# Performance work log

Hardware: AMD Instinct MI355X
Metric: run time of the kernel (lower is better)

## Reference

```python
import jax, jax.numpy as jnp
import numpy as np

EPS = 1e-8
TAU = 1.0
ROLL_TOPK = 20
FINAL_TOPK = 20


def _ln(x, g, b):
    mu = x.mean(-1, keepdims=True)
    var = ((x - mu) ** 2).mean(-1, keepdims=True)
    return (x - mu) / jnp.sqrt(var + 1e-5) * g + b


def _row_norm(A, pm):
    A = A * pm
    return A / (A.sum(-1, keepdims=True) + EPS)


def _topk_sparsify(A, k, pm):
    thr = jax.lax.top_k(A, k)[0][..., -1:]  # per-row k-th largest
    return _row_norm(jnp.where(A >= thr, A, 0.0), pm)


def setup_inputs():
    key = jax.random.key(0)
    ks = iter(jax.random.split(key, 48))
    B, N, Din, Dh, T, R, Bn = 4, 2000, 128, 256, 64, 16, 64
    def w(shape, s=0.02):
        return jax.random.normal(next(ks), shape, jnp.float32) * s
    inp = dict(
        X=jax.random.normal(next(ks), (B, N, Din), jnp.float32),
        mask=jnp.ones((B, N), dtype=bool),
        history=jax.random.normal(next(ks), (B, N, T), jnp.float32),
        enc_ln_g=jnp.ones((Din,)), enc_ln_b=jnp.zeros((Din,)),
        enc_w1=w((Din, Bn)), enc_b1=jnp.zeros((Bn,)),
        enc_w2=w((Bn, Din)), enc_b2=jnp.zeros((Din,)),
        proj_w=w((Din, Dh)), proj_b=jnp.zeros((Dh,)),
        fdg_B=w((R, Din), 0.1),
        mix_logit=jnp.asarray(np.log(0.7 / 0.3), dtype=jnp.float32),
        gblk_ln_g=jnp.ones((Dh,)), gblk_ln_b=jnp.zeros((Dh,)),
        gblk_w1=w((Dh, Dh)), gblk_b1=jnp.zeros((Dh,)),
        gblk_w2=w((Dh, Dh)), gblk_b2=jnp.zeros((Dh,)),
        head_ln_g=jnp.ones((Dh,)), head_ln_b=jnp.zeros((Dh,)),
        head_w=w((Dh, 1)), head_b=jnp.zeros((1,)),
    )
    for i in range(2):  # residual_layers=2
        inp[f'blk{i}_ln_g'] = jnp.ones((Dh,))
        inp[f'blk{i}_ln_b'] = jnp.zeros((Dh,))
        inp[f'blk{i}_w1'] = w((Dh, Dh))
        inp[f'blk{i}_b1'] = jnp.zeros((Dh,))
        inp[f'blk{i}_w2'] = w((Dh, Dh))
        inp[f'blk{i}_b2'] = jnp.zeros((Dh,))
    return inp


def _forward(X, mask, history, enc_ln_g, enc_ln_b, enc_w1, enc_b1, enc_w2, enc_b2,
             proj_w, proj_b,
             blk0_ln_g, blk0_ln_b, blk0_w1, blk0_b1, blk0_w2, blk0_b2,
             blk1_ln_g, blk1_ln_b, blk1_w1, blk1_b1, blk1_w2, blk1_b2,
             fdg_B, mix_logit,
             gblk_ln_g, gblk_ln_b, gblk_w1, gblk_b1, gblk_w2, gblk_b2,
             head_ln_g, head_ln_b, head_w, head_b):
    m = mask.astype(X.dtype)[..., None]                      # [B,N,1]
    pm = (mask[:, :, None] & mask[:, None, :]).astype(X.dtype)  # [B,N,N]
    # FeatureBottleneck encoder (residual down-up projection)
    h = _ln(X, enc_ln_g, enc_ln_b)
    Xm = (X + jax.nn.gelu(h @ enc_w1 + enc_b1) @ enc_w2 + enc_b2) * m
    hid = (Xm @ proj_w + proj_b) * m
    # ResidualMLP blocks
    for (g, bb, w1, b1, w2, b2) in ((blk0_ln_g, blk0_ln_b, blk0_w1, blk0_b1, blk0_w2, blk0_b2),
                                    (blk1_ln_g, blk1_ln_b, blk1_w1, blk1_b1, blk1_w2, blk1_b2)):
        hh = _ln(hid, g, bb)
        hid = (hid + jax.nn.gelu(hh @ w1 + b1) @ w2 + b2) * m
    # FDG: low-rank cosine-similarity graph with temperature softmax
    Z = Xm @ fdg_B.T                                          # [B,N,R]
    Zn = Z / (jnp.linalg.norm(Z, axis=-1, keepdims=True) + EPS)
    S = jnp.einsum('bnr,bmr->bnm', Zn, Zn) / TAU
    A_fdg = jax.nn.softmax(jnp.where(pm > 0, S, -1e9), axis=-1) * pm
    # Rolling correlation graph from history returns
    Hc = history - history.mean(-1, keepdims=True)
    Hn = Hc / (Hc.std(-1, keepdims=True) + EPS)
    C = jnp.einsum('bnt,bmt->bnm', Hn, Hn) / history.shape[-1]
    A_roll = _topk_sparsify(_row_norm(jax.nn.relu(C), pm), ROLL_TOPK, pm)
    # Mix -> row-normalize -> final top-k sparsify
    mix = jax.nn.sigmoid(mix_logit)
    A = _row_norm(mix * A_fdg + (1.0 - mix) * A_roll, pm)
    A = _topk_sparsify(A, FINAL_TOPK, pm)
    # GraphResidual block: aggregate then MLP with residual
    hh = _ln(hid, gblk_ln_g, gblk_ln_b)
    msg = jnp.einsum('bnm,bmd->bnd', A, hh)
    hid = (hid + jax.nn.gelu(msg @ gblk_w1 + gblk_b1) @ gblk_w2 + gblk_b2) * m
    # Head
    y = (jax.nn.gelu(_ln(hid, head_ln_g, head_ln_b)) @ head_w + head_b)[..., 0]
    return jnp.where(mask, y, 0.0)


def reference(X, mask, history, enc_ln_g, enc_ln_b, enc_w1, enc_b1, enc_w2, enc_b2,
              proj_w, proj_b,
              blk0_ln_g, blk0_ln_b, blk0_w1, blk0_b1, blk0_w2, blk0_b2,
              blk1_ln_g, blk1_ln_b, blk1_w1, blk1_b1, blk1_w2, blk1_b2,
              fdg_B, mix_logit,
              gblk_ln_g, gblk_ln_b, gblk_w1, gblk_b1, gblk_w2, gblk_b2,
              head_ln_g, head_ln_b, head_w, head_b):
    return _forward(X, mask, history, enc_ln_g, enc_ln_b, enc_w1, enc_b1, enc_w2, enc_b2,
                    proj_w, proj_b,
                    blk0_ln_g, blk0_ln_b, blk0_w1, blk0_b1, blk0_w2, blk0_b2,
                    blk1_ln_g, blk1_ln_b, blk1_w1, blk1_b1, blk1_w2, blk1_b2,
                    fdg_B, mix_logit,
                    gblk_ln_g, gblk_ln_b, gblk_w1, gblk_b1, gblk_w2, gblk_b2,
                    head_ln_g, head_ln_b, head_w, head_b)
```

## Files before the change

kernel.cpp:

```cpp
#include <hip/hip_runtime.h>
#include <math.h>

#define NB 4
#define N 2000
#define DIN 128
#define DH 256
#define NROWS (NB*N)
#define EPSF 1e-8f

typedef __attribute__((ext_vector_type(8))) short bf16x8;
typedef __attribute__((ext_vector_type(4))) float f32x4;


__device__ __forceinline__ float gelu_t(float x){
    float z = 0.7978845608028654f * fmaf(0.044715f * x * x, x, x);
    z = fminf(fmaxf(z, -20.f), 20.f);
    float e = __expf(2.f * z);
    return 0.5f * x * (1.f + (e - 1.f) / (e + 1.f));
}

__device__ __forceinline__ unsigned short f2bf(float f){
    unsigned u = __float_as_uint(f);
    return (unsigned short)((u + 0x7FFFu + ((u >> 16) & 1u)) >> 16);
}

__device__ __forceinline__ float wave_sort64_desc(float v){
    const int lane = threadIdx.x & 63;
    #pragma unroll
    for (int k = 2; k <= 64; k <<= 1){
        #pragma unroll
        for (int j = k >> 1; j >= 1; j >>= 1){
            float o = __shfl_xor(v, j, 64);
            bool keepMax = ((lane & k) == 0) == ((lane & j) == 0);
            v = keepMax ? fmaxf(v, o) : fminf(v, o);
        }
    }
    return v;
}

__device__ __forceinline__ void sort128_desc(float &v0, float &v1){
    const int lane = threadIdx.x & 63;
    #pragma unroll
    for (int k = 2; k <= 128; k <<= 1){
        #pragma unroll
        for (int j = k >> 1; j >= 2; j >>= 1){
            int lj = j >> 1;
            float o0 = __shfl_xor(v0, lj, 64);
            float o1 = __shfl_xor(v1, lj, 64);
            int idx0 = 2*lane, idx1 = 2*lane + 1;
            bool km0 = ((idx0 & k) == 0) == ((idx0 & j) == 0);
            bool km1 = ((idx1 & k) == 0) == ((idx1 & j) == 0);
            v0 = km0 ? fmaxf(v0, o0) : fminf(v0, o0);
            v1 = km1 ? fmaxf(v1, o1) : fminf(v1, o1);
        }
        {
            bool up = (((2*lane) & k) == 0);
            float a = fmaxf(v0, v1), b = fminf(v0, v1);
            v0 = up ? a : b;
            v1 = up ? b : a;
        }
    }
}

__device__ __forceinline__ float wave_topk20_slow32(const float (&v)[32]){
    float cur = 1e30f, kth = 0.f;
    int consumed = 0;
    for (int it = 0; it < 20; ++it){
        if (consumed >= 20) break;
        float bm = -3.f;
        #pragma unroll
        for (int i = 0; i < 32; ++i){ if (v[i] < cur) bm = fmaxf(bm, v[i]); }
        #pragma unroll
        for (int mm = 1; mm < 64; mm <<= 1) bm = fmaxf(bm, __shfl_xor(bm, mm, 64));
        int c = 0;
        #pragma unroll
        for (int i = 0; i < 32; ++i) c += (v[i] == bm) ? 1 : 0;
        #pragma unroll
        for (int mm = 1; mm < 64; mm <<= 1) c += __shfl_xor(c, mm, 64);
        consumed += c;
        kth = bm;
        cur = bm;
    }
    return kth;
}

__device__ __forceinline__ float wave_topk20_sync(const float (&v)[32], float* cl){
    const int lane = threadIdx.x & 63;
    float mx = v[0];
    #pragma unroll
    for (int i = 1; i < 32; ++i) mx = fmaxf(mx, v[i]);
    float sm = wave_sort64_desc(mx);
    float u = __shfl(sm, 19, 64);
    int cnt = 0;
    #pragma unroll
    for (int i = 0; i < 32; ++i) cnt += (v[i] >= u) ? 1 : 0;
    int incl = cnt;
    #pragma unroll
    for (int s = 1; s < 64; s <<= 1){
        int o = __shfl_up(incl, s, 64);
        if (lane >= s) incl += o;
    }
    const int total = __shfl(incl, 63, 64);
    const bool fast = (total <= 128);
    if (fast){
        int offs = incl - cnt;
        #pragma unroll
        for (int i = 0; i < 32; ++i){
            if (v[i] >= u) cl[offs++] = v[i];
        }
    }
    __syncthreads();
    float kth;
    if (fast){
        float c0 = (2*lane     < total) ? cl[2*lane]     : -3.f;
        float c1 = (2*lane + 1 < total) ? cl[2*lane + 1] : -3.f;
        sort128_desc(c0, c1);
        kth = __shfl(c1, 9, 64);
    } else {
        kth = wave_topk20_slow32(v);
    }
    __syncthreads();
    return kth;
}

__device__ __forceinline__ void mfma_gemm16(
    const unsigned short (*__restrict__ sA)[264], const unsigned short* __restrict__ Wt,
    int l15, int hi, int cbase, f32x4 acc[4])
{
    bf16x8 a[8];
    #pragma unroll
    for (int kb = 0; kb < 8; ++kb)
        a[kb] = *(const bf16x8*)&sA[l15][kb*32 + hi*8];
    __syncthreads();
    const unsigned short* wp0 = Wt + (size_t)(cbase      + l15)*256 + hi*8;
    const unsigned short* wp1 = Wt + (size_t)(cbase + 16 + l15)*256 + hi*8;
    const unsigned short* wp2 = Wt + (size_t)(cbase + 32 + l15)*256 + hi*8;
    const unsigned short* wp3 = Wt + (size_t)(cbase + 48 + l15)*256 + hi*8;
    #pragma unroll
    for (int kb = 0; kb < 8; ++kb){
        bf16x8 b0 = *(const bf16x8*)(wp0 + kb*32);
        bf16x8 b1 = *(const bf16x8*)(wp1 + kb*32);
        bf16x8 b2 = *(const bf16x8*)(wp2 + kb*32);
        bf16x8 b3 = *(const bf16x8*)(wp3 + kb*32);
        acc[0] = __builtin_amdgcn_mfma_f32_16x16x32_bf16(a[kb], b0, acc[0], 0, 0, 0);
        acc[1] = __builtin_amdgcn_mfma_f32_16x16x32_bf16(a[kb], b1, acc[1], 0, 0, 0);
        acc[2] = __builtin_amdgcn_mfma_f32_16x16x32_bf16(a[kb], b2, acc[2], 0, 0, 0);
        acc[3] = __builtin_amdgcn_mfma_f32_16x16x32_bf16(a[kb], b3, acc[3], 0, 0, 0);
    }
}


__global__ __launch_bounds__(256) void k_wcvt(
    const float* __restrict__ w10, const float* __restrict__ w20,
    const float* __restrict__ w11, const float* __restrict__ w21,
    const float* __restrict__ gw1, const float* __restrict__ gw2,
    unsigned short* __restrict__ Wt)
{
    __shared__ float t[32][33];
    const int m = blockIdx.z;
    const float* W = (m==0)?w10:(m==1)?w20:(m==2)?w11:(m==3)?w21:(m==4)?gw1:gw2;
    unsigned short* out = Wt + (size_t)m*65536;
    const int k0 = blockIdx.y*32, c0 = blockIdx.x*32;
    const int tx = threadIdx.x & 31, ty = threadIdx.x >> 5;
    #pragma unroll
    for (int j = 0; j < 4; ++j){
        int k = ty*4 + j;
        t[k][tx] = W[(size_t)(k0+k)*256 + c0+tx];
    }
    __syncthreads();
    #pragma unroll
    for (int j = 0; j < 4; ++j){
        int c = ty*4 + j;
        out[(size_t)(c0+c)*256 + k0+tx] = f2bf(t[tx][c]);
    }
}

__global__ __launch_bounds__(256) void k_enc(
    const float* __restrict__ X,
    const float* __restrict__ lg, const float* __restrict__ lb,
    const float* __restrict__ w1, const float* __restrict__ b1,
    const float* __restrict__ w2, const float* __restrict__ b2,
    const float* __restrict__ pw, const float* __restrict__ pb,
    const float* __restrict__ fB,
    float* __restrict__ hid, float* __restrict__ Zn)
{
    __shared__ float sH[8][132];
    __shared__ float sT[8][68];
    __shared__ float sXm[8][132];
    const int tid = threadIdx.x;
    const int lane = tid & 63;
    const int wave = tid >> 6;
    const int rg = wave * 2;
    const int row0 = blockIdx.x * 8;
    const int cx = lane * 2;
    float2 x0 = *(const float2*)(X + (size_t)(row0+rg  )*128 + cx);
    float2 x1 = *(const float2*)(X + (size_t)(row0+rg+1)*128 + cx);
    {
        float sa = x0.x + x0.y, sb = x1.x + x1.y;
        float qa = x0.x*x0.x + x0.y*x0.y, qb = x1.x*x1.x + x1.y*x1.y;
        #pragma unroll
        for (int m = 1; m < 64; m <<= 1){
            sa += __shfl_xor(sa, m, 64); sb += __shfl_xor(sb, m, 64);
            qa += __shfl_xor(qa, m, 64); qb += __shfl_xor(qb, m, 64);
        }
        float mua = sa*(1.f/128.f), mub = sb*(1.f/128.f);
        float rsa = rsqrtf(qa*(1.f/128.f) - mua*mua + 1e-5f);
        float rsb = rsqrtf(qb*(1.f/128.f) - mub*mub + 1e-5f);
        float2 gg = *(const float2*)(lg + cx);
        float2 bb = *(const float2*)(lb + cx);
        sH[rg  ][cx] = (x0.x - mua)*rsa*gg.x + bb.x;
        sH[rg  ][cx+1] = (x0.y - mua)*rsa*gg.y + bb.y;
        sH[rg+1][cx] = (x1.x - mub)*rsb*gg.x + bb.x;
        sH[rg+1][cx+1] = (x1.y - mub)*rsb*gg.y + bb.y;
    }
    __syncthreads();
    {
        float a0 = 0.f, a1 = 0.f;
        #pragma unroll 4
        for (int k = 0; k < 128; ++k){
            float h0 = sH[rg][k], h1 = sH[rg+1][k];
            float wk = w1[k*64 + lane];
            a0 = fmaf(h0, wk, a0);
            a1 = fmaf(h1, wk, a1);
        }
        float bb = b1[lane];
        sT[rg  ][lane] = gelu_t(a0 + bb);
        sT[rg+1][lane] = gelu_t(a1 + bb);
    }
    __syncthreads();
    {
        float p0x=0.f,p0y=0.f,p1x=0.f,p1y=0.f;
        #pragma unroll 4
        for (int k = 0; k < 64; ++k){
            float t0 = sT[rg][k], t1 = sT[rg+1][k];
            float2 w = *(const float2*)(w2 + k*128 + cx);
            p0x = fmaf(t0, w.x, p0x); p0y = fmaf(t0, w.y, p0y);
            p1x = fmaf(t1, w.x, p1x); p1y = fmaf(t1, w.y, p1y);
        }
        float2 bb = *(const float2*)(b2 + cx);
        sXm[rg  ][cx]   = x0.x + p0x + bb.x;
        sXm[rg  ][cx+1] = x0.y + p0y + bb.y;
        sXm[rg+1][cx]   = x1.x + p1x + bb.x;
        sXm[rg+1][cx+1] = x1.y + p1y + bb.y;
    }
    __syncthreads();
    {
        const int ri = lane >> 4;
        const int wc = wave*64 + (lane & 15)*4;
        float a0[4] = {0,0,0,0}, a1[4] = {0,0,0,0};
        #pragma unroll 4
        for (int k = 0; k < 128; ++k){
            float h0 = sXm[ri*2][k], h1 = sXm[ri*2+1][k];
            float4 w = *(const float4*)(pw + k*256 + wc);
            a0[0]=fmaf(h0,w.x,a0[0]); a0[1]=fmaf(h0,w.y,a0[1]); a0[2]=fmaf(h0,w.z,a0[2]); a0[3]=fmaf(h0,w.w,a0[3]);
            a1[0]=fmaf(h1,w.x,a1[0]); a1[1]=fmaf(h1,w.y,a1[1]); a1[2]=fmaf(h1,w.z,a1[2]); a1[3]=fmaf(h1,w.w,a1[3]);
        }
        float4 bb = *(const float4*)(pb + wc);
        float4 o0 = make_float4(a0[0]+bb.x, a0[1]+bb.y, a0[2]+bb.z, a0[3]+bb.w);
        float4 o1 = make_float4(a1[0]+bb.x, a1[1]+bb.y, a1[2]+bb.z, a1[3]+bb.w);
        *(float4*)(hid + (size_t)(row0+ri*2  )*256 + wc) = o0;
        *(float4*)(hid + (size_t)(row0+ri*2+1)*256 + wc) = o1;
    }
    if (tid < 128){
        const int r = tid >> 4, q = tid & 15;
        float z = 0.f;
        #pragma unroll 4
        for (int k = 0; k < 128; ++k) z = fmaf(sXm[r][k], fB[q*128 + k], z);
        float s2 = z*z;
        #pragma unroll
        for (int m = 1; m < 16; m <<= 1) s2 += __shfl_xor(s2, m, 64);
        Zn[(size_t)(row0 + r)*16 + q] = z / (sqrtf(s2) + EPSF);
    }
}

__global__ __launch_bounds__(256) void k_hist(const float* __restrict__ H, float* __restrict__ HnT)
{
    const int row  = blockIdx.x * 4 + (threadIdx.x >> 6);
    const int lane = threadIdx.x & 63;
    float v = H[(size_t)row*64 + lane];
    float s = v;
    #pragma unroll
    for (int mm = 1; mm < 64; mm <<= 1) s += __shfl_xor(s, mm, 64);
    float mu = s * (1.f/64.f);
    float d = v - mu;
    float s2 = d*d;
    #pragma unroll
    for (int mm = 1; mm < 64; mm <<= 1) s2 += __shfl_xor(s2, mm, 64);
    float sd = sqrtf(s2 * (1.f/64.f));
    const int b = row / N, nloc = row % N;
    HnT[(size_t)b*64*N + (size_t)lane*N + nloc] = d / ((sd + EPSF) * 8.f);
}

__global__ __launch_bounds__(256) void k_mlp2(
    float* __restrict__ hid, const unsigned short* __restrict__ Wtb,
    const float* __restrict__ g0, const float* __restrict__ be0,
    const float* __restrict__ b10, const float* __restrict__ b20,
    const float* __restrict__ g1, const float* __restrict__ be1,
    const float* __restrict__ b11, const float* __restrict__ b21,
    const float* __restrict__ hg, const float* __restrict__ hb,
    float* __restrict__ hh_out)
{
    __shared__ float sR[16][264];
    __shared__ unsigned short sA[16][264];
    const int tid = threadIdx.x;
    const int lane = tid & 63, wave = tid >> 6;
    const int l15 = lane & 15, hi = lane >> 4;
    const int cbase = wave * 64;
    const int row0 = blockIdx.x * 16;
    {
        const int r = tid >> 4, cb = (tid & 15) * 4;
        #pragma unroll
        for (int q = 0; q < 4; ++q)
            *(float4*)&sR[r][cb + q*64] =
                *(const float4*)(hid + (size_t)(row0+r)*256 + cb + q*64);
    }
    __syncthreads();
    #pragma unroll
    for (int it = 0; it < 2; ++it){
        const float* g  = it ? g1  : g0;
        const float* be = it ? be1 : be0;
        const float* B1 = it ? b11 : b10;
        const float* B2 = it ? b21 : b20;
        const unsigned short* W1 = Wtb + (size_t)(it ? 2 : 0)*65536;
        const unsigned short* W2 = Wtb + (size_t)(it ? 3 : 1)*65536;
        {
            float4 gg = *(const float4*)(g + lane*4);
            float4 bb = *(const float4*)(be + lane*4);
            #pragma unroll
            for (int j = 0; j < 4; ++j){
                const int r = wave*4 + j;
                float4 v = *(const float4*)&sR[r][lane*4];
                float s = v.x+v.y+v.z+v.w;
                float q = v.x*v.x+v.y*v.y+v.z*v.z+v.w*v.w;
                #pragma unroll
                for (int m = 1; m < 64; m <<= 1){
                    s += __shfl_xor(s, m, 64); q += __shfl_xor(q, m, 64);
                }
                float mu = s*(1.f/256.f);
                float rs = rsqrtf(q*(1.f/256.f) - mu*mu + 1e-5f);
                ushort4 o;
                o.x = f2bf((v.x-mu)*rs*gg.x+bb.x);
                o.y = f2bf((v.y-mu)*rs*gg.y+bb.y);
                o.z = f2bf((v.z-mu)*rs*gg.z+bb.z);
                o.w = f2bf((v.w-mu)*rs*gg.w+bb.w);
                *(ushort4*)&sA[r][lane*4] = o;
            }
        }
        __syncthreads();
        {
            f32x4 acc[4];
            #pragma unroll
            for (int t = 0; t < 4; ++t){ acc[t][0]=0.f; acc[t][1]=0.f; acc[t][2]=0.f; acc[t][3]=0.f; }
            mfma_gemm16(sA, W1, l15, hi, cbase, acc);
            #pragma unroll
            for (int t = 0; t < 4; ++t){
                int ct = cbase + t*16 + l15;
                float bbx = B1[ct];
                #pragma unroll
                for (int j = 0; j < 4; ++j)
                    sA[hi*4 + j][ct] = f2bf(gelu_t(acc[t][j] + bbx));
            }
        }
        __syncthreads();
        {
            f32x4 acc[4];
            #pragma unroll
            for (int t = 0; t < 4; ++t){ acc[t][0]=0.f; acc[t][1]=0.f; acc[t][2]=0.f; acc[t][3]=0.f; }
            mfma_gemm16(sA, W2, l15, hi, cbase, acc);
            #pragma unroll
            for (int t = 0; t < 4; ++t){
                int ct = cbase + t*16 + l15;
                float bbx = B2[ct];
                #pragma unroll
                for (int j = 0; j < 4; ++j)
                    sR[hi*4 + j][ct] += acc[t][j] + bbx;
            }
        }
        __syncthreads();
    }
    {
        const int r = tid >> 4, cb = (tid & 15) * 4;
        #pragma unroll
        for (int q = 0; q < 4; ++q)
            *(float4*)(hid + (size_t)(row0+r)*256 + cb + q*64) =
                *(const float4*)&sR[r][cb + q*64];
    }
    {
        float4 gg = *(const float4*)(hg + lane*4);
        float4 bb = *(const float4*)(hb + lane*4);
        #pragma unroll
        for (int j = 0; j < 4; ++j){
            const int r = wave*4 + j;
            float4 v = *(const float4*)&sR[r][lane*4];
            float s = v.x+v.y+v.z+v.w;
            float q = v.x*v.x+v.y*v.y+v.z*v.z+v.w*v.w;
            #pragma unroll
            for (int m = 1; m < 64; m <<= 1){
                s += __shfl_xor(s, m, 64); q += __shfl_xor(q, m, 64);
            }
            float mu = s*(1.f/256.f);
            float rs = rsqrtf(q*(1.f/256.f) - mu*mu + 1e-5f);
            float4 o = make_float4((v.x-mu)*rs*gg.x+bb.x, (v.y-mu)*rs*gg.y+bb.y,
                                   (v.z-mu)*rs*gg.z+bb.z, (v.w-mu)*rs*gg.w+bb.w);
            *(float4*)(hh_out + (size_t)(row0+r)*256 + lane*4) = o;
        }
    }
}

__global__ __launch_bounds__(256) void k_corr(const float* __restrict__ HnTc,
                                              float* __restrict__ rcb)
{
    __shared__ float sA[64][32];
    __shared__ float sB[64][128];
    const int tid = threadIdx.x;
    const float* H = HnTc + (size_t)blockIdx.z * 64 * N;
    float* rc = rcb + (size_t)blockIdx.z * N * N;
    const int n0 = blockIdx.x * 32;
    const int cs = blockIdx.y * 512;
    const int ce = (cs + 512 < N) ? cs + 512 : N;
    #pragma unroll
    for (int j = 0; j < 8; ++j){
        int idx = tid + 256*j;
        int k = idx >> 5, r = idx & 31;
        int nn = n0 + r;
        sA[k][r] = (nn < N) ? H[(size_t)k*N + nn] : 0.f;
    }
    const int trow = tid >> 6;
    const int tcol = tid & 63;
    for (int mc = cs; mc < ce; mc += 128){
        __syncthreads();
        #pragma unroll
        for (int q = 0; q < 8; ++q){
            int f = tid + 256*q;
            int k = f >> 5, c4 = (f & 31) * 4;
            int m = mc + c4;
            float4 v = (m + 3 < N) ? *(const float4*)(H + (size_t)k*N + m)
                                   : make_float4(0.f,0.f,0.f,0.f);
            *(float4*)&sB[k][c4] = v;
        }
        __syncthreads();
        float acc[8][2];
        #pragma unroll
        for (int r = 0; r < 8; ++r){ acc[r][0] = 0.f; acc[r][1] = 0.f; }
        #pragma unroll 4
        for (int k = 0; k < 64; ++k){
            float2 b2v = *(const float2*)&sB[k][tcol*2];
            float4 a0 = *(const float4*)&sA[k][trow*8];
            float4 a1 = *(const float4*)&sA[k][trow*8 + 4];
            float av[8] = {a0.x,a0.y,a0.z,a0.w,a1.x,a1.y,a1.z,a1.w};
            #pragma unroll
            for (int r = 0; r < 8; ++r){
                acc[r][0] = fmaf(av[r], b2v.x, acc[r][0]);
                acc[r][1] = fmaf(av[r], b2v.y, acc[r][1]);
            }
        }
        int m = mc + tcol*2;
        if (m < N){
            #pragma unroll
            for (int r = 0; r < 8; ++r){
                int nn = n0 + trow*8 + r;
                if (nn < N){
                    float2 o = make_float2(fmaxf(acc[r][0],0.f), fmaxf(acc[r][1],0.f));
                    *(float2*)(rc + (size_t)nn*N + m) = o;
                }
            }
        }
    }
}

__global__ __launch_bounds__(256) void k_select(
    const float* __restrict__ rcb, const float* __restrict__ Zn,
    const float* __restrict__ hh, const float* __restrict__ mix_logit,
    float* __restrict__ msg, int row_base)
{
    __shared__ float cl[4][128];
    __shared__ int   lm[4][64];
    __shared__ float lv[4][64];
    const int tid = threadIdx.x;
    const int lane = tid & 63, wv = tid >> 6;
    const int rloc = blockIdx.x * 4 + wv;
    const int n = row_base + rloc;
    const int base = (n / N) * N;
    const float* rcrow = rcb + (size_t)rloc * N;
    float* clw = cl[wv];
    float zr[16];
    {
        const float4* zp = (const float4*)(Zn + (size_t)n * 16);
        float4 z0 = zp[0], z1 = zp[1], z2 = zp[2], z3 = zp[3];
        zr[0]=z0.x; zr[1]=z0.y; zr[2]=z0.z; zr[3]=z0.w;
        zr[4]=z1.x; zr[5]=z1.y; zr[6]=z1.z; zr[7]=z1.w;
        zr[8]=z2.x; zr[9]=z2.y; zr[10]=z2.z; zr[11]=z2.w;
        zr[12]=z3.x; zr[13]=z3.y; zr[14]=z3.z; zr[15]=z3.w;
    }
    float e_[32], rc_[32];
    float sumE = 0.f, sumC = 0.f;
    #pragma unroll
    for (int i = 0; i < 32; ++i){
        const int m = lane + 64*i;
        float rcv = -1.f, e = 0.f;
        if (m < N){
            rcv = rcrow[m];
            const float4* zp = (const float4*)(Zn + (size_t)(base + m) * 16);
            float4 za = zp[0], zb = zp[1], zc = zp[2], zd = zp[3];
            float s = za.x * zr[0];
            s = fmaf(za.y, zr[1], s);  s = fmaf(za.z, zr[2], s);  s = fmaf(za.w, zr[3], s);
            s = fmaf(zb.x, zr[4], s);  s = fmaf(zb.y, zr[5], s);  s = fmaf(zb.z, zr[6], s);
            s = fmaf(zb.w, zr[7], s);  s = fmaf(zc.x, zr[8], s);  s = fmaf(zc.y, zr[9], s);
            s = fmaf(zc.z, zr[10], s); s = fmaf(zc.w, zr[11], s); s = fmaf(zd.x, zr[12], s);
            s = fmaf(zd.y, zr[13], s); s = fmaf(zd.z, zr[14], s); s = fmaf(zd.w, zr[15], s);
            e = __expf(s);
            sumE += e; sumC += rcv;
        }
        e_[i] = e; rc_[i] = rcv;
    }
    #pragma unroll
    for (int mm = 1; mm < 64; mm <<= 1){
        sumE += __shfl_xor(sumE, mm, 64);
        sumC += __shfl_xor(sumC, mm, 64);
    }
    float c_kth = wave_topk20_sync(rc_, clw);
    float skl = 0.f;
    #pragma unroll
    for (int i = 0; i < 32; ++i){ if (rc_[i] >= c_kth) skl += rc_[i]; }
    #pragma unroll
    for (int mm = 1; mm < 64; mm <<= 1) skl += __shfl_xor(skl, mm, 64);
    const float invSumExp = 1.f / sumE;
    const float r1 = 1.f / (sumC + EPSF);
    const float rollsc = r1 * (1.f / (skl * r1 + EPSF));
    const float mixw = 1.f / (1.f + __expf(-mix_logit[0]));
    const float onemix = 1.f - mixw;
    float sumAm = 0.f;
    #pragma unroll
    for (int i = 0; i < 32; ++i){
        float am = -1.f;
        if (rc_[i] >= 0.f){
            float afdg  = e_[i] * invSumExp;
            float aroll = (rc_[i] >= c_kth) ? rc_[i] * rollsc : 0.f;
            am = fmaf(mixw, afdg, onemix * aroll);
            sumAm += am;
        }
        e_[i] = am;
    }
    #pragma unroll
    for (int mm = 1; mm < 64; mm <<= 1) sumAm += __shfl_xor(sumAm, mm, 64);
    float am_kth = wave_topk20_sync(e_, clw);
    float sk2 = 0.f;
    #pragma unroll
    for (int i = 0; i < 32; ++i){ if (e_[i] >= am_kth) sk2 += e_[i]; }
    #pragma unroll
    for (int mm = 1; mm < 64; mm <<= 1) sk2 += __shfl_xor(sk2, mm, 64);
    const float ra = 1.f / (sumAm + EPSF);
    const float fsc = ra * (1.f / (sk2 * ra + EPSF));
    unsigned keep = 0; int cnt = 0;
    #pragma unroll
    for (int i = 0; i < 32; ++i){
        bool kp = (e_[i] >= am_kth) && (e_[i] > 0.f);
        if (kp){ keep |= (1u << i); cnt++; }
    }
    int incl = cnt;
    #pragma unroll
    for (int s = 1; s < 64; s <<= 1){
        int o = __shfl_up(incl, s, 64);
        if (lane >= s) incl += o;
    }
    int total = __shfl(incl, 63, 64);
    if (total > 64) total = 64;
    int offs = incl - cnt;
    #pragma unroll
    for (int i = 0; i < 32; ++i){
        if (keep & (1u << i)){
            if (offs < 64){ lm[wv][offs] = lane + 64*i; lv[wv][offs] = e_[i] * fsc; }
            offs++;
        }
    }
    __syncthreads();
    float a0 = 0.f, a1 = 0.f, a2 = 0.f, a3 = 0.f;
    for (int i = 0; i < total; ++i){
        float w = lv[wv][i];
        const float4 hv = *(const float4*)(hh + ((size_t)(base + lm[wv][i]))*256 + lane*4);
        a0 = fmaf(w, hv.x, a0); a1 = fmaf(w, hv.y, a1);
        a2 = fmaf(w, hv.z, a2); a3 = fmaf(w, hv.w, a3);
    }
    *(float4*)(msg + (size_t)n*256 + lane*4) = make_float4(a0, a1, a2, a3);
}

__global__ __launch_bounds__(256) void k_gblk(
    const float* __restrict__ hid, const float* __restrict__ msgb,
    const unsigned short* __restrict__ Wtb,
    const float* __restrict__ b1, const float* __restrict__ b2,
    const float* __restrict__ hg, const float* __restrict__ hb,
    const float* __restrict__ hw, const float* __restrict__ hbias,
    float* __restrict__ y)
{
    __shared__ float sR[16][264];
    __shared__ unsigned short sA[16][264];
    const int tid = threadIdx.x;
    const int lane = tid & 63, wave = tid >> 6;
    const int l15 = lane & 15, hi = lane >> 4;
    const int cbase = wave * 64;
    const int row0 = blockIdx.x * 16;
    {
        const int r = tid >> 4, cb = (tid & 15) * 4;
        #pragma unroll
        for (int q = 0; q < 4; ++q){
            *(float4*)&sR[r][cb + q*64] =
                *(const float4*)(hid + (size_t)(row0+r)*256 + cb + q*64);
            float4 mv = *(const float4*)(msgb + (size_t)(row0+r)*256 + cb + q*64);
            ushort4 u;
            u.x = f2bf(mv.x); u.y = f2bf(mv.y); u.z = f2bf(mv.z); u.w = f2bf(mv.w);
            *(ushort4*)&sA[r][cb + q*64] = u;
        }
    }
    __syncthreads();
    {
        f32x4 acc[4];
        #pragma unroll
        for (int t = 0; t < 4; ++t){ acc[t][0]=0.f; acc[t][1]=0.f; acc[t][2]=0.f; acc[t][3]=0.f; }
        mfma_gemm16(sA, Wtb + (size_t)4*65536, l15, hi, cbase, acc);
        #pragma unroll
        for (int t = 0; t < 4; ++t){
            int ct = cbase + t*16 + l15;
            float bbx = b1[ct];
            #pragma unroll
            for (int j = 0; j < 4; ++j)
                sA[hi*4 + j][ct] = f2bf(gelu_t(acc[t][j] + bbx));
        }
    }
    __syncthreads();
    {
        f32x4 acc[4];
        #pragma unroll
        for (int t = 0; t < 4; ++t){ acc[t][0]=0.f; acc[t][1]=0.f; acc[t][2]=0.f; acc[t][3]=0.f; }
        mfma_gemm16(sA, Wtb + (size_t)5*65536, l15, hi, cbase, acc);
        #pragma unroll
        for (int t = 0; t < 4; ++t){
            int ct = cbase + t*16 + l15;
            float bbx = b2[ct];
            #pragma unroll
            for (int j = 0; j < 4; ++j)
                sR[hi*4 + j][ct] += acc[t][j] + bbx;
        }
    }
    __syncthreads();
    {
        float4 gg = *(const float4*)(hg + lane*4);
        float4 bb = *(const float4*)(hb + lane*4);
        float4 wv = *(const float4*)(hw + lane*4);
        #pragma unroll
        for (int j = 0; j < 4; ++j){
            const int r = wave*4 + j;
            float4 v = *(const float4*)&sR[r][lane*4];
            float s = v.x+v.y+v.z+v.w;
            float q = v.x*v.x+v.y*v.y+v.z*v.z+v.w*v.w;
            #pragma unroll
            for (int m = 1; m < 64; m <<= 1){
                s += __shfl_xor(s, m, 64); q += __shfl_xor(q, m, 64);
            }
            float mu = s*(1.f/256.f);
            float rs = rsqrtf(q*(1.f/256.f) - mu*mu + 1e-5f);
            float p = gelu_t((v.x-mu)*rs*gg.x+bb.x)*wv.x
                    + gelu_t((v.y-mu)*rs*gg.y+bb.y)*wv.y
                    + gelu_t((v.z-mu)*rs*gg.z+bb.z)*wv.z
                    + gelu_t((v.w-mu)*rs*gg.w+bb.w)*wv.w;
            #pragma unroll
            for (int m = 1; m < 64; m <<= 1) p += __shfl_xor(p, m, 64);
            if (lane == 0) y[row0 + r] = p + hbias[0];
        }
    }
}


extern "C" void kernel_launch(void* const* d_in, const int* in_sizes, int n_in,
                              void* d_out, int out_size, void* d_ws, size_t ws_size,
                              hipStream_t stream)
{
    (void)in_sizes; (void)n_in; (void)out_size;
    const float* X         = (const float*)d_in[0];
    const float* history   = (const float*)d_in[2];
    const float* enc_ln_g  = (const float*)d_in[3];
    const float* enc_ln_b  = (const float*)d_in[4];
    const float* enc_w1    = (const float*)d_in[5];
    const float* enc_b1    = (const float*)d_in[6];
    const float* enc_w2    = (const float*)d_in[7];
    const float* enc_b2    = (const float*)d_in[8];
    const float* proj_w    = (const float*)d_in[9];
    const float* proj_b    = (const float*)d_in[10];
    const float* fdg_B     = (const float*)d_in[11];
    const float* mixlog    = (const float*)d_in[12];
    const float* gblk_ln_g = (const float*)d_in[13];
    const float* gblk_ln_b = (const float*)d_in[14];
    const float* gblk_w1   = (const float*)d_in[15];
    const float* gblk_b1   = (const float*)d_in[16];
    const float* gblk_w2   = (const float*)d_in[17];
    const float* gblk_b2   = (const float*)d_in[18];
    const float* head_ln_g = (const float*)d_in[19];
    const float* head_ln_b = (const float*)d_in[20];
    const float* head_w    = (const float*)d_in[21];
    const float* head_b    = (const float*)d_in[22];

    float* ws  = (float*)d_ws;
    float* hid = ws;
    float* hh  = hid + (size_t)NROWS*DH;
    float* msg = hh  + (size_t)NROWS*DH;
    float* Znb = msg + (size_t)NROWS*DH;
    float* HnT = Znb + (size_t)NROWS*16;
    unsigned short* Wtb = (unsigned short*)(HnT + (size_t)NB*64*N);
    float* rcbuf = (float*)(Wtb + (size_t)6*65536);
    float* y   = (float*)d_out;

    const size_t baseF = (size_t)3*NROWS*DH + (size_t)NROWS*16 + (size_t)NB*64*N
                       + (size_t)6*65536/2;
    const size_t perBatchF = (size_t)N*N;
    size_t availF = (ws_size/4 > baseF) ? (ws_size/4 - baseF) : perBatchF;
    int bpc = (availF >= 4*perBatchF) ? 4 : (availF >= 2*perBatchF) ? 2 : 1;

    k_wcvt<<<dim3(8,8,6), 256, 0, stream>>>(
        (const float*)d_in[25], (const float*)d_in[27],
        (const float*)d_in[31], (const float*)d_in[33],
        gblk_w1, gblk_w2, Wtb);
    k_enc<<<NROWS/8, 256, 0, stream>>>(X, enc_ln_g, enc_ln_b, enc_w1, enc_b1, enc_w2, enc_b2,
                                       proj_w, proj_b, fdg_B, hid, Znb);
    k_hist<<<NROWS/4, 256, 0, stream>>>(history, HnT);
    k_mlp2<<<NROWS/16, 256, 0, stream>>>(hid, Wtb,
        (const float*)d_in[23], (const float*)d_in[24],
        (const float*)d_in[26], (const float*)d_in[28],
        (const float*)d_in[29], (const float*)d_in[30],
        (const float*)d_in[32], (const float*)d_in[34],
        gblk_ln_g, gblk_ln_b, hh);
    for (int cb = 0; cb < NB; cb += bpc){
        dim3 g1(63, 4, bpc);
        k_corr<<<g1, 256, 0, stream>>>(HnT + (size_t)cb*64*N, rcbuf);
        k_select<<<bpc*N/4, 256, 0, stream>>>(rcbuf, Znb, hh, mixlog, msg, cb*N);
    }
    k_gblk<<<NROWS/16, 256, 0, stream>>>(hid, msg, Wtb, gblk_b1, gblk_b2,
                                         head_ln_g, head_ln_b, head_w, head_b, y);
}
```

Before: 240.1 us.

## Split each k_select row across two waves with shared-memory cross-wave reductions

k_select now assigns one row per 128-thread block (two waves) instead of one row per wave, halving the per-thread register arrays from 32 to 16 and adding shared-memory exchanges plus barriers for sums, top-k thresholds and compaction offsets. The query vector is loaded via readfirstlane so it sits in scalar registers. The aim is lower register pressure and higher occupancy for this latency-bound selection kernel. The cost is extra __syncthreads per row, and the gather now uses float2 loads instead of float4.

```diff
diff --git a/kernel.cpp b/kernel.cpp
--- a/kernel.cpp
+++ b/kernel.cpp
@@ -62,50 +62,62 @@
     }
 }
 
-__device__ __forceinline__ float wave_topk20_slow32(const float (&v)[32]){
+__device__ __forceinline__ float topk20_slow_2w(const float (&v)[16],
+        float* wu, int* wcnt)
+{
+    const int lane = threadIdx.x & 63, wv = threadIdx.x >> 6;
     float cur = 1e30f, kth = 0.f;
     int consumed = 0;
     for (int it = 0; it < 20; ++it){
-        if (consumed >= 20) break;
         float bm = -3.f;
         #pragma unroll
-        for (int i = 0; i < 32; ++i){ if (v[i] < cur) bm = fmaxf(bm, v[i]); }
+        for (int i = 0; i < 16; ++i){ if (v[i] < cur) bm = fmaxf(bm, v[i]); }
         #pragma unroll
         for (int mm = 1; mm < 64; mm <<= 1) bm = fmaxf(bm, __shfl_xor(bm, mm, 64));
+        if (lane == 0) wu[wv] = bm;
+        __syncthreads();
+        bm = fmaxf(wu[0], wu[1]);
         int c = 0;
         #pragma unroll
-        for (int i = 0; i < 32; ++i) c += (v[i] == bm) ? 1 : 0;
+        for (int i = 0; i < 16; ++i) c += (v[i] == bm) ? 1 : 0;
         #pragma unroll
         for (int mm = 1; mm < 64; mm <<= 1) c += __shfl_xor(c, mm, 64);
-        consumed += c;
-        kth = bm;
-        cur = bm;
+        if (lane == 0) wcnt[wv] = c;
+        __syncthreads();
+        c = wcnt[0] + wcnt[1];
+        if (consumed < 20){ consumed += c; kth = bm; cur = bm; }
     }
     return kth;
 }
 
-__device__ __forceinline__ float wave_topk20_sync(const float (&v)[32], float* cl){
-    const int lane = threadIdx.x & 63;
+__device__ __forceinline__ float topk20_2w(const float (&v)[16],
+        float* cl, float* wu, int* wcnt)
+{
+    const int lane = threadIdx.x & 63, wv = threadIdx.x >> 6;
     float mx = v[0];
     #pragma unroll
-    for (int i = 1; i < 32; ++i) mx = fmaxf(mx, v[i]);
+    for (int i = 1; i < 16; ++i) mx = fmaxf(mx, v[i]);
     float sm = wave_sort64_desc(mx);
-    float u = __shfl(sm, 19, 64);
+    if (lane == 19) wu[wv] = sm;
+    __syncthreads();
+    const float u = fmaxf(wu[0], wu[1]);
     int cnt = 0;
     #pragma unroll
-    for (int i = 0; i < 32; ++i) cnt += (v[i] >= u) ? 1 : 0;
+    for (int i = 0; i < 16; ++i) cnt += (v[i] >= u) ? 1 : 0;
     int incl = cnt;
     #pragma unroll
     for (int s = 1; s < 64; s <<= 1){
         int o = __shfl_up(incl, s, 64);
         if (lane >= s) incl += o;
     }
-    const int total = __shfl(incl, 63, 64);
+    if (lane == 63) wcnt[wv] = incl;
+    __syncthreads();
+    const int total = wcnt[0] + wcnt[1];
     const bool fast = (total <= 128);
     if (fast){
-        int offs = incl - cnt;
-        #pragma unroll
-        for (int i = 0; i < 32; ++i){
+        int offs = incl - cnt + (wv ? wcnt[0] : 0);
+        #pragma unroll
+        for (int i = 0; i < 16; ++i){
             if (v[i] >= u) cl[offs++] = v[i];
         }
     }
@@ -117,7 +129,7 @@
         sort128_desc(c0, c1);
         kth = __shfl(c1, 9, 64);
     } else {
-        kth = wave_topk20_slow32(v);
+        kth = topk20_slow_2w(v, wu, wcnt);
     }
     __syncthreads();
     return kth;
@@ -468,35 +480,35 @@
     }
 }
 
-__global__ __launch_bounds__(256) void k_select(
+__global__ __launch_bounds__(128, 8) void k_select(
     const float* __restrict__ rcb, const float* __restrict__ Zn,
     const float* __restrict__ hh, const float* __restrict__ mix_logit,
     float* __restrict__ msg, int row_base)
 {
-    __shared__ float cl[4][128];
-    __shared__ int   lm[4][64];
-    __shared__ float lv[4][64];
+    __shared__ float cl[128];
+    __shared__ float xch[2][6];
+    __shared__ float wu[2];
+    __shared__ int   wcnt[2];
+    __shared__ int   lm[64];
+    __shared__ float lv[64];
     const int tid = threadIdx.x;
     const int lane = tid & 63, wv = tid >> 6;
-    const int rloc = blockIdx.x * 4 + wv;
+    const int rloc = blockIdx.x;
     const int n = row_base + rloc;
     const int base = (n / N) * N;
     const float* rcrow = rcb + (size_t)rloc * N;
-    float* clw = cl[wv];
     float zr[16];
     {
-        const float4* zp = (const float4*)(Zn + (size_t)n * 16);
-        float4 z0 = zp[0], z1 = zp[1], z2 = zp[2], z3 = zp[3];
-        zr[0]=z0.x; zr[1]=z0.y; zr[2]=z0.z; zr[3]=z0.w;
-        zr[4]=z1.x; zr[5]=z1.y; zr[6]=z1.z; zr[7]=z1.w;
-        zr[8]=z2.x; zr[9]=z2.y; zr[10]=z2.z; zr[11]=z2.w;
-        zr[12]=z3.x; zr[13]=z3.y; zr[14]=z3.z; zr[15]=z3.w;
-    }
-    float e_[32], rc_[32];
+        const float* zp = Zn + (size_t)n * 16;
+        #pragma unroll
+        for (int q = 0; q < 16; ++q)
+            zr[q] = __uint_as_float(__builtin_amdgcn_readfirstlane(__float_as_uint(zp[q])));
+    }
+    float e_[16], rc_[16];
     float sumE = 0.f, sumC = 0.f;
     #pragma unroll
-    for (int i = 0; i < 32; ++i){
-        const int m = lane + 64*i;
+    for (int i = 0; i < 16; ++i){
+        const int m = tid + 128*i;
         float rcv = -1.f, e = 0.f;
         if (m < N){
             rcv = rcrow[m];
@@ -518,12 +530,18 @@
         sumE += __shfl_xor(sumE, mm, 64);
         sumC += __shfl_xor(sumC, mm, 64);
     }
-    float c_kth = wave_topk20_sync(rc_, clw);
+    if (lane == 0){ xch[wv][0] = sumE; xch[wv][1] = sumC; }
+    float c_kth = topk20_2w(rc_, cl, wu, wcnt);
+    sumE = xch[0][0] + xch[1][0];
+    sumC = xch[0][1] + xch[1][1];
     float skl = 0.f;
     #pragma unroll
-    for (int i = 0; i < 32; ++i){ if (rc_[i] >= c_kth) skl += rc_[i]; }
+    for (int i = 0; i < 16; ++i){ if (rc_[i] >= c_kth) skl += rc_[i]; }
     #pragma unroll
     for (int mm = 1; mm < 64; mm <<= 1) skl += __shfl_xor(skl, mm, 64);
+    if (lane == 0) xch[wv][2] = skl;
+    __syncthreads();
+    skl = xch[0][2] + xch[1][2];
     const float invSumExp = 1.f / sumE;
     const float r1 = 1.f / (sumC + EPSF);
     const float rollsc = r1 * (1.f / (skl * r1 + EPSF));
@@ -531,7 +549,7 @@
     const float onemix = 1.f - mixw;
     float sumAm = 0.f;
     #pragma unroll
-    for (int i = 0; i < 32; ++i){
+    for (int i = 0; i < 16; ++i){
         float am = -1.f;
         if (rc_[i] >= 0.f){
             float afdg  = e_[i] * invSumExp;
@@ -543,17 +561,22 @@
     }
     #pragma unroll
     for (int mm = 1; mm < 64; mm <<= 1) sumAm += __shfl_xor(sumAm, mm, 64);
-    float am_kth = wave_topk20_sync(e_, clw);
+    if (lane == 0) xch[wv][3] = sumAm;
+    float am_kth = topk20_2w(e_, cl, wu, wcnt);
+    sumAm = xch[0][3] + xch[1][3];
     float sk2 = 0.f;
     #pragma unroll
-    for (int i = 0; i < 32; ++i){ if (e_[i] >= am_kth) sk2 += e_[i]; }
+    for (int i = 0; i < 16; ++i){ if (e_[i] >= am_kth) sk2 += e_[i]; }
     #pragma unroll
     for (int mm = 1; mm < 64; mm <<= 1) sk2 += __shfl_xor(sk2, mm, 64);
+    if (lane == 0) xch[wv][4] = sk2;
+    __syncthreads();
+    sk2 = xch[0][4] + xch[1][4];
     const float ra = 1.f / (sumAm + EPSF);
     const float fsc = ra * (1.f / (sk2 * ra + EPSF));
     unsigned keep = 0; int cnt = 0;
     #pragma unroll
-    for (int i = 0; i < 32; ++i){
+    for (int i = 0; i < 16; ++i){
         bool kp = (e_[i] >= am_kth) && (e_[i] > 0.f);
         if (kp){ keep |= (1u << i); cnt++; }
     }
@@ -563,25 +586,27 @@
         int o = __shfl_up(incl, s, 64);
         if (lane >= s) incl += o;
     }
-    int total = __shfl(incl, 63, 64);
+    if (lane == 63) wcnt[wv] = incl;
+    __syncthreads();
+    int total = wcnt[0] + wcnt[1];
     if (total > 64) total = 64;
-    int offs = incl - cnt;
-    #pragma unroll
-    for (int i = 0; i < 32; ++i){
+    int offs = incl - cnt + (wv ? wcnt[0] : 0);
+    #pragma unroll
+    for (int i = 0; i < 16; ++i){
         if (keep & (1u << i)){
-            if (offs < 64){ lm[wv][offs] = lane + 64*i; lv[wv][offs] = e_[i] * fsc; }
+            if (offs < 64){ lm[offs] = tid + 128*i; lv[offs] = e_[i] * fsc; }
             offs++;
         }
     }
     __syncthreads();
-    float a0 = 0.f, a1 = 0.f, a2 = 0.f, a3 = 0.f;
+    const int d0 = tid * 2;
+    float a0 = 0.f, a1 = 0.f;
     for (int i = 0; i < total; ++i){
-        float w = lv[wv][i];
-        const float4 hv = *(const float4*)(hh + ((size_t)(base + lm[wv][i]))*256 + lane*4);
+        float w = lv[i];
+        const float2 hv = *(const float2*)(hh + ((size_t)(base + lm[i]))*256 + d0);
         a0 = fmaf(w, hv.x, a0); a1 = fmaf(w, hv.y, a1);
-        a2 = fmaf(w, hv.z, a2); a3 = fmaf(w, hv.w, a3);
-    }
-    *(float4*)(msg + (size_t)n*256 + lane*4) = make_float4(a0, a1, a2, a3);
+    }
+    *(float2*)(msg + (size_t)n*256 + d0) = make_float2(a0, a1);
 }
 
 __global__ __launch_bounds__(256) void k_gblk(
@@ -730,7 +755,7 @@
     for (int cb = 0; cb < NB; cb += bpc){
         dim3 g1(63, 4, bpc);
         k_corr<<<g1, 256, 0, stream>>>(HnT + (size_t)cb*64*N, rcbuf);
-        k_select<<<bpc*N/4, 256, 0, stream>>>(rcbuf, Znb, hh, mixlog, msg, cb*N);
+        k_select<<<bpc*N, 128, 0, stream>>>(rcbuf, Znb, hh, mixlog, msg, cb*N);
     }
     k_gblk<<<NROWS/16, 256, 0, stream>>>(hid, msg, Wtb, gblk_b1, gblk_b2,
                                          head_ln_g, head_ln_b, head_w, head_b, y);
```

After: 248.1 us. +3.3%, slower.
